# Kernel tuning notes

Measured on AMD Instinct MI355X. Metric: run time of the kernel, lower is better.

## Reference

```python
import jax, jax.numpy as jnp
import numpy as np

TRAJ_LEN = 25      # save points, as in the original module
N_SUB = 8          # fixed Tsit5 substeps per save interval (replaces adaptive PID stepping)
BATCH = 524288

# Tsit5 Butcher tableau (Tsitouras 2011), same method diffrax.Tsit5 uses.
A21 = 0.161
A31, A32 = -0.008480655492356989, 0.335480655492357
A41, A42, A43 = 2.8971530571054935, -6.359448489975075, 4.3622954328695815
A51, A52, A53, A54 = 5.325864828439257, -11.748883564062828, 7.4955393428898365, -0.09249506636175525
A61, A62, A63, A64, A65 = 5.86145544294642, -12.92096931784711, 8.159367898576159, -0.071584973281401, -0.028269050394068383
# 5th-order solution weights (b == a7j, FSAL)
B1, B2, B3, B4, B5, B6 = 0.09646076681806523, 0.01, 0.4798896504144996, 1.379008574103742, -3.290069515436081, 2.324710524099774


def setup_inputs() -> dict:
    key = jax.random.key(0)
    k1, k2 = jax.random.split(key)
    x0s = jax.random.normal(k1, (BATCH, 2), dtype=jnp.float32)
    matrix = 0.1 * jax.random.normal(k2, (2, 2), dtype=jnp.float32)
    T = jnp.float32(2.0)
    return {"x0s": x0s, "matrix": matrix, "T": T}


def reference(x0s, matrix, T):
    # dx/dt = T * (matrix @ x); integrate on t in [0,1], save at 25 equispaced times.
    h = jnp.float32(1.0 / ((TRAJ_LEN - 1) * N_SUB))

    def f(y):  # batched vector field: [B,2] @ [2,2]^T
        return T * (y @ matrix.T)

    def tsit5_step(y):
        k1 = f(y)
        k2 = f(y + h * (A21 * k1))
        k3 = f(y + h * (A31 * k1 + A32 * k2))
        k4 = f(y + h * (A41 * k1 + A42 * k2 + A43 * k3))
        k5 = f(y + h * (A51 * k1 + A52 * k2 + A53 * k3 + A54 * k4))
        k6 = f(y + h * (A61 * k1 + A62 * k2 + A63 * k3 + A64 * k4 + A65 * k5))
        return y + h * (B1 * k1 + B2 * k2 + B3 * k3 + B4 * k4 + B5 * k5 + B6 * k6)

    def interval(y, _):
        def sub(yy, __):
            return tsit5_step(yy), None
        y, _ = jax.lax.scan(sub, y, None, length=N_SUB)
        return y, y

    _, ys = jax.lax.scan(interval, x0s, None, length=TRAJ_LEN - 1)  # [24,B,2]
    trajs = jnp.concatenate([x0s[:, None, :], jnp.moveaxis(ys, 0, 1)], axis=1)  # [B,25,2]
    num_steps = jnp.int32(x0s.shape[0] * (TRAJ_LEN - 1) * N_SUB)  # total steps analog of sum(num_steps)
    return trajs, num_steps
```

## Files before the change

### kernel.cpp

```cpp
#include <hip/hip_runtime.h>

#define TRAJ_LEN 25
#define N_SUB 8

#define CA21 0.161
#define CA31 -0.008480655492356989
#define CA32 0.335480655492357
#define CA41 2.8971530571054935
#define CA42 -6.359448489975075
#define CA43 4.3622954328695815
#define CA51 5.325864828439257
#define CA52 -11.748883564062828
#define CA53 7.4955393428898365
#define CA54 -0.09249506636175525
#define CA61 5.86145544294642
#define CA62 -12.92096931784711
#define CA63 8.159367898576159
#define CA64 -0.071584973281401
#define CA65 -0.028269050394068383
#define CB1 0.09646076681806523
#define CB2 0.01
#define CB3 0.4798896504144996
#define CB4 1.379008574103742
#define CB5 -3.290069515436081
#define CB6 2.324710524099774

struct M2 { double a, b, c, d; };

__device__ __forceinline__ M2 mmul(const M2& x, const M2& y) {
    return { x.a * y.a + x.b * y.c, x.a * y.b + x.b * y.d,
             x.c * y.a + x.d * y.c, x.c * y.b + x.d * y.d };
}
__device__ __forceinline__ M2 msc(double s, const M2& x) {
    return { s * x.a, s * x.b, s * x.c, s * x.d };
}
__device__ __forceinline__ M2 madd(const M2& x, const M2& y) {
    return { x.a + y.a, x.b + y.b, x.c + y.c, x.d + y.d };
}
__device__ __forceinline__ M2 eyeph(double h, const M2& x) {
    return { 1.0 + h * x.a, h * x.b, h * x.c, 1.0 + h * x.d };
}

__global__ __launch_bounds__(256) void ode_kernel(
        const float* __restrict__ x0s, const float* __restrict__ mat,
        const float* __restrict__ Tp, float* __restrict__ out,
        int batch, int nthreads, int out_last) {
    const int tid = blockIdx.x * 256 + threadIdx.x;

    const double T = (double)Tp[0];
    const double h = (double)(float)(1.0 / ((TRAJ_LEN - 1) * N_SUB));
    const M2 A = { T * (double)mat[0], T * (double)mat[1],
                   T * (double)mat[2], T * (double)mat[3] };

    M2 S1 = A;
    M2 S2 = mmul(A, eyeph(h, msc(CA21, S1)));
    M2 S3 = mmul(A, eyeph(h, madd(msc(CA31, S1), msc(CA32, S2))));
    M2 S4 = mmul(A, eyeph(h, madd(madd(msc(CA41, S1), msc(CA42, S2)), msc(CA43, S3))));
    M2 S5 = mmul(A, eyeph(h, madd(madd(madd(msc(CA51, S1), msc(CA52, S2)), msc(CA53, S3)), msc(CA54, S4))));
    M2 S6 = mmul(A, eyeph(h, madd(madd(madd(madd(msc(CA61, S1), msc(CA62, S2)), msc(CA63, S3)), msc(CA64, S4)), msc(CA65, S5))));
    M2 S = eyeph(h, madd(madd(madd(madd(madd(msc(CB1, S1), msc(CB2, S2)), msc(CB3, S3)), msc(CB4, S4)), msc(CB5, S5)), msc(CB6, S6)));
    M2 G2 = mmul(S, S);
    M2 G4 = mmul(G2, G2);
    M2 G8 = mmul(G4, G4);

    const float g00 = (float)G8.a, g01 = (float)G8.b;
    const float g10 = (float)G8.c, g11 = (float)G8.d;

    if (tid < nthreads) {
        #pragma unroll
        for (int k = 0; k < 4; ++k) {
            const int e = tid + k * nthreads;
            if (e >= batch) break;
            const float2 p = ((const float2*)x0s)[e];
            float y0 = p.x, y1 = p.y;
            float2* o = (float2*)(out + (size_t)e * (TRAJ_LEN * 2));
            o[0] = p;
            #pragma unroll
            for (int i = 1; i < TRAJ_LEN; ++i) {
                const float n0 = fmaf(g00, y0, g01 * y1);
                const float n1 = fmaf(g10, y0, g11 * y1);
                y0 = n0; y1 = n1;
                o[i] = make_float2(y0, y1);
            }
        }
    }

    if (tid == 0) {
        out[out_last] = (float)((long long)batch * (TRAJ_LEN - 1) * N_SUB);
    }
}

extern "C" void kernel_launch(void* const* d_in, const int* in_sizes, int n_in,
                              void* d_out, int out_size, void* d_ws, size_t ws_size,
                              hipStream_t stream) {
    const float* x0s = (const float*)d_in[0];
    const float* mat = (const float*)d_in[1];
    const float* T   = (const float*)d_in[2];
    float* out = (float*)d_out;

    const int batch = in_sizes[0] / 2;
    const int EPT = 4;
    const int nthreads = (batch + EPT - 1) / EPT;
    const int blocks = (nthreads + 255) / 256;

    hipLaunchKernelGGL(ode_kernel, dim3(blocks), dim3(256), 0, stream,
                       x0s, mat, T, out, batch, nthreads, out_size - 1);
}
```

Before: 138.6 us.

## Precompute propagator powers once and write trajectories with coalesced float4 stores

Adds a single-thread setup kernel that builds the 25 powers of the 8-substep Tsit5 propagator matrix into workspace. A second kernel maps each thread to two consecutive output points (one float4) and computes them with direct matrix-vector products instead of a per-element serial recurrence. The aim is fully coalesced, vectorized output stores in place of the old strided per-trajectory writes. The cost is an extra kernel launch with a serial setup and integer divisions per thread. Using precomputed powers instead of repeated float multiplication also changes rounding slightly.

```diff
diff --git a/kernel.cpp b/kernel.cpp
--- a/kernel.cpp
+++ b/kernel.cpp
@@ -41,11 +41,12 @@
     return { 1.0 + h * x.a, h * x.b, h * x.c, 1.0 + h * x.d };
 }
 
-__global__ __launch_bounds__(256) void ode_kernel(
-        const float* __restrict__ x0s, const float* __restrict__ mat,
-        const float* __restrict__ Tp, float* __restrict__ out,
-        int batch, int nthreads, int out_last) {
-    const int tid = blockIdx.x * 256 + threadIdx.x;
+__global__ void setup_kernel(const float* __restrict__ mat,
+                             const float* __restrict__ Tp,
+                             float4* __restrict__ gpow,
+                             float* __restrict__ out, int out_last,
+                             float nsteps) {
+    if (threadIdx.x != 0 || blockIdx.x != 0) return;
 
     const double T = (double)Tp[0];
     const double h = (double)(float)(1.0 / ((TRAJ_LEN - 1) * N_SUB));
@@ -61,33 +62,42 @@
     M2 S = eyeph(h, madd(madd(madd(madd(madd(msc(CB1, S1), msc(CB2, S2)), msc(CB3, S3)), msc(CB4, S4)), msc(CB5, S5)), msc(CB6, S6)));
     M2 G2 = mmul(S, S);
     M2 G4 = mmul(G2, G2);
-    M2 G8 = mmul(G4, G4);
+    M2 G  = mmul(G4, G4);
 
-    const float g00 = (float)G8.a, g01 = (float)G8.b;
-    const float g10 = (float)G8.c, g11 = (float)G8.d;
+    M2 P = { 1.0, 0.0, 0.0, 1.0 };
+    #pragma unroll 1
+    for (int i = 0; i < TRAJ_LEN; ++i) {
+        gpow[i] = make_float4((float)P.a, (float)P.b, (float)P.c, (float)P.d);
+        P = mmul(G, P);
+    }
+    out[out_last] = nsteps;
+}
 
-    if (tid < nthreads) {
-        #pragma unroll
-        for (int k = 0; k < 4; ++k) {
-            const int e = tid + k * nthreads;
-            if (e >= batch) break;
-            const float2 p = ((const float2*)x0s)[e];
-            float y0 = p.x, y1 = p.y;
-            float2* o = (float2*)(out + (size_t)e * (TRAJ_LEN * 2));
-            o[0] = p;
-            #pragma unroll
-            for (int i = 1; i < TRAJ_LEN; ++i) {
-                const float n0 = fmaf(g00, y0, g01 * y1);
-                const float n1 = fmaf(g10, y0, g11 * y1);
-                y0 = n0; y1 = n1;
-                o[i] = make_float2(y0, y1);
-            }
-        }
-    }
+__global__ __launch_bounds__(256) void traj_kernel(
+        const float2* __restrict__ x0,
+        const float4* __restrict__ gpow,
+        float4* __restrict__ out, int n4) {
+    const int t = blockIdx.x * 256 + threadIdx.x;
+    if (t >= n4) return;
 
-    if (tid == 0) {
-        out[out_last] = (float)((long long)batch * (TRAJ_LEN - 1) * N_SUB);
-    }
+    const int o0 = 2 * t;
+    const int o1 = o0 + 1;
+    const int e0 = o0 / TRAJ_LEN;
+    const int i0 = o0 - e0 * TRAJ_LEN;
+    const int e1 = o1 / TRAJ_LEN;
+    const int i1 = o1 - e1 * TRAJ_LEN;
+
+    const float4 g0 = gpow[i0];
+    const float4 g1 = gpow[i1];
+    const float2 p0 = x0[e0];
+    const float2 p1 = x0[e1];
+
+    const float r0x = fmaf(g0.x, p0.x, g0.y * p0.y);
+    const float r0y = fmaf(g0.z, p0.x, g0.w * p0.y);
+    const float r1x = fmaf(g1.x, p1.x, g1.y * p1.y);
+    const float r1y = fmaf(g1.z, p1.x, g1.w * p1.y);
+
+    out[t] = make_float4(r0x, r0y, r1x, r1y);
 }
 
 extern "C" void kernel_launch(void* const* d_in, const int* in_sizes, int n_in,
@@ -97,12 +107,18 @@
     const float* mat = (const float*)d_in[1];
     const float* T   = (const float*)d_in[2];
     float* out = (float*)d_out;
+    float4* gpow = (float4*)d_ws;
 
     const int batch = in_sizes[0] / 2;
-    const int EPT = 4;
-    const int nthreads = (batch + EPT - 1) / EPT;
-    const int blocks = (nthreads + 255) / 256;
+    const long long nsteps = (long long)batch * (TRAJ_LEN - 1) * N_SUB;
 
-    hipLaunchKernelGGL(ode_kernel, dim3(blocks), dim3(256), 0, stream,
-                       x0s, mat, T, out, batch, nthreads, out_size - 1);
+    const int traj_floats = batch * TRAJ_LEN * 2;
+    const int n4 = traj_floats / 4;
+    const int blocks = (n4 + 255) / 256;
+
+    hipLaunchKernelGGL(setup_kernel, dim3(1), dim3(64), 0, stream,
+                       mat, T, gpow, out, out_size - 1, (float)nsteps);
+    hipLaunchKernelGGL(traj_kernel, dim3(blocks), dim3(256), 0, stream,
+                       (const float2*)x0s, (const float4*)gpow,
+                       (float4*)out, n4);
 }
```

Result: faster. 132.6 us (-4.4%).
